# Kernel optimization log

Measured on AMD Instinct MI355X. Metric: run time of the kernel, lower is better.

The kernel has to match this reference:

```python
import jax, jax.numpy as jnp
import numpy as np

N_NODES = 100000
N_EDGES = 1600000
IN_CH, HID_CH, OUT_CH = 128, 128, 64


def _sage_conv(x, src, dst, deg_inv, W_l, b_l, W_r):
    # PyG SAGEConv (mean aggr): out = lin_l(mean_{j in N(i)} x_j) + lin_r(x_i)
    msg = x[src]                                   # [E, C_in] gather
    agg = jax.ops.segment_sum(msg, dst, num_segments=N_NODES)  # [N, C_in]
    agg = agg * deg_inv[:, None]
    return agg @ W_l.T + b_l + x @ W_r.T


def setup_inputs() -> dict:
    key = jax.random.key(0)
    ks = jax.random.split(key, 10)
    x = jax.random.normal(ks[0], (N_NODES, IN_CH), dtype=jnp.float32)
    edge_attr = jax.random.normal(ks[1], (N_EDGES, 4), dtype=jnp.float32)
    edge_index = jax.random.randint(ks[2], (2, N_EDGES), 0, N_NODES, dtype=jnp.int32)
    dims = [(IN_CH, HID_CH), (HID_CH, HID_CH), (HID_CH, OUT_CH)]
    params = {}
    for i, (cin, cout) in enumerate(dims):
        s = 1.0 / np.sqrt(cin)
        params[f"W_l{i}"] = jax.random.uniform(ks[3 + 2 * i], (cout, cin), minval=-s, maxval=s, dtype=jnp.float32)
        params[f"b_l{i}"] = jnp.zeros((cout,), dtype=jnp.float32)
        params[f"W_r{i}"] = jax.random.uniform(ks[4 + 2 * i], (cout, cin), minval=-s, maxval=s, dtype=jnp.float32)
    return {"x": x, "edge_attr": edge_attr, "edge_index": edge_index, **params}


def reference(x, edge_attr, edge_index,
              W_l0, b_l0, W_r0,
              W_l1, b_l1, W_r1,
              W_l2, b_l2, W_r2):
    src, dst = edge_index[0], edge_index[1]
    deg = jax.ops.segment_sum(jnp.ones((N_EDGES,), jnp.float32), dst, num_segments=N_NODES)
    deg_inv = 1.0 / jnp.maximum(deg, 1.0)
    layers = [(W_l0, b_l0, W_r0), (W_l1, b_l1, W_r1), (W_l2, b_l2, W_r2)]
    h = x
    for i, (Wl, bl, Wr) in enumerate(layers):
        h = _sage_conv(h, src, dst, deg_inv, Wl, bl, Wr)
        if i != len(layers) - 1:
            h = jax.nn.relu(h)
            # dropout is identity in eval mode (training=False)
    return h
```

## Files before the change

kernel.cpp:

```cpp
#include <hip/hip_runtime.h>
#include <cstdint>

#define N_NODES 100000
#define N_EDGES 1600000

constexpr int NCB = 196;
constexpr int HB  = 391;

typedef __attribute__((ext_vector_type(8))) short short8;
typedef __attribute__((ext_vector_type(4))) float f32x4;

__device__ inline uint32_t fbits(float f) { union { float f; uint32_t u; } c; c.f = f; return c.u; }
__device__ inline float bfloat(uint32_t u) { union { uint32_t u; float f; } c; c.u = u; return c.f; }

__device__ inline void bsplit(float a, short& hi, short& lo) {
    uint32_t h = fbits(a) & 0xFFFF0000u;
    float fl = a - bfloat(h);
    hi = (short)(h >> 16);
    lo = (short)(fbits(fl) >> 16);
}

__device__ inline ushort f2bf(float f) {
    uint32_t u = fbits(f);
    return (ushort)((u + 0x7FFFu + ((u >> 16) & 1u)) >> 16);
}


__global__ __launch_bounds__(256)
void hist_kernel(const int* __restrict__ dst, int* __restrict__ H) {
    __shared__ int h[NCB];
    for (int i = threadIdx.x; i < NCB; i += 256) h[i] = 0;
    __syncthreads();
    int e0 = blockIdx.x * 4096;
    #pragma unroll
    for (int it = 0; it < 16; ++it) {
        int e = e0 + it * 256 + threadIdx.x;
        if (e < N_EDGES) atomicAdd(&h[dst[e] >> 9], 1);
    }
    __syncthreads();
    for (int i = threadIdx.x; i < NCB; i += 256) H[blockIdx.x * NCB + i] = h[i];
}

__global__ __launch_bounds__(256)
void scanbase_kernel(int* __restrict__ H, int* __restrict__ boff) {
    __shared__ int tot[NCB];
    __shared__ int base[NCB + 1];
    int j = threadIdx.x;
    if (j < NCB) {
        int s = 0;
        for (int b = 0; b < HB; ++b) s += H[b * NCB + j];
        tot[j] = s;
    }
    __syncthreads();
    if (j == 0) {
        int run = 0;
        for (int k = 0; k < NCB; ++k) { base[k] = run; run += tot[k]; }
        base[NCB] = run;
    }
    __syncthreads();
    if (j <= NCB) boff[j] = base[j];
    if (j < NCB) {
        int run = base[j];
        for (int b = 0; b < HB; ++b) {
            int v = H[b * NCB + j];
            H[b * NCB + j] = run;
            run += v;
        }
    }
}

__global__ __launch_bounds__(256)
void scatter_kernel(const int* __restrict__ src, const int* __restrict__ dst,
                    const int* __restrict__ H, uint32_t* __restrict__ ebuf) {
    __shared__ int cur[NCB];
    for (int i = threadIdx.x; i < NCB; i += 256) cur[i] = H[blockIdx.x * NCB + i];
    __syncthreads();
    int e0 = blockIdx.x * 4096;
    #pragma unroll
    for (int it = 0; it < 16; ++it) {
        int e = e0 + it * 256 + threadIdx.x;
        if (e < N_EDGES) {
            int d = dst[e];
            int p = atomicAdd(&cur[d >> 9], 1);
            ebuf[p] = ((uint32_t)src[e] << 9) | (uint32_t)(d & 511);
        }
    }
}


__global__ __launch_bounds__(256)
void bucket_csr(const uint32_t* __restrict__ ebuf, const int* __restrict__ boff,
                int* __restrict__ off, float* __restrict__ dinv,
                int* __restrict__ ssrc) {
    __shared__ int deg[512];
    __shared__ int cur[512];
    __shared__ int wsum[4];
    int t = threadIdx.x, lane = t & 63, w = t >> 6;
    int j = blockIdx.x;
    int base = boff[j], end = boff[j + 1];
    int node0 = j << 9;

    deg[t] = 0; deg[t + 256] = 0;
    __syncthreads();

    for (int p = base + t; p < end; p += 256)
        atomicAdd(&deg[ebuf[p] & 511u], 1);
    __syncthreads();

    int d0 = deg[2 * t], d1 = deg[2 * t + 1];
    int s = d0 + d1;
    int incl = s;
    #pragma unroll
    for (int d = 1; d < 64; d <<= 1) {
        int u = __shfl_up(incl, d);
        if (lane >= d) incl += u;
    }
    if (lane == 63) wsum[w] = incl;
    __syncthreads();
    if (t < 4) {
        int v = wsum[t];
        int iv = v;
        #pragma unroll
        for (int d = 1; d < 4; d <<= 1) {
            int u = __shfl_up(iv, d, 4);
            if (t >= d) iv += u;
        }
        wsum[t] = iv - v;
    }
    __syncthreads();
    int ebase = wsum[w] + (incl - s);
    cur[2 * t] = ebase;
    cur[2 * t + 1] = ebase + d0;
    int n0 = node0 + 2 * t, n1 = n0 + 1;
    if (n0 < N_NODES) {
        off[n0] = base + ebase;
        dinv[n0] = 1.0f / (float)max(d0, 1);
    }
    if (n1 < N_NODES) {
        off[n1] = base + ebase + d0;
        dinv[n1] = 1.0f / (float)max(d1, 1);
    }
    if (j == 0 && t == 0) off[N_NODES] = N_EDGES;
    __syncthreads();

    for (int p = base + t; p < end; p += 256) {
        uint32_t ent = ebuf[p];
        int pos = atomicAdd(&cur[ent & 511u], 1);
        ssrc[base + pos] = (int)(ent >> 9);
    }
}


__global__ void wfrag_kernel(const float* __restrict__ W1, const float* __restrict__ W2,
                             int C1, int NCT, int ntask,
                             short* __restrict__ fhi, short* __restrict__ flo) {
    int tau = blockIdx.x * 256 + threadIdx.x;
    if (tau >= ntask) return;
    int lane = tau & 63;
    int ct = (tau >> 6) % NCT;
    int ks = (tau >> 6) / NCT;
    int col = ct * 16 + (lane & 15);
    int k = ks * 32 + (lane >> 4) * 8;
    const float* p = (col < C1) ? &W1[(size_t)col * 128 + k]
                                : &W2[(size_t)(col - C1) * 128 + k];
    short8 h8, l8;
    #pragma unroll
    for (int j = 0; j < 8; ++j) {
        short h, l;
        bsplit(p[j], h, l);
        h8[j] = h; l8[j] = l;
    }
    *reinterpret_cast<short8*>(&fhi[(size_t)tau * 8]) = h8;
    *reinterpret_cast<short8*>(&flo[(size_t)tau * 8]) = l8;
}


template<int C1, int C2>
__global__ __launch_bounds__(256)
void gemm_f32(const float* __restrict__ H, const short* __restrict__ Wfhi,
              const short* __restrict__ Wflo, const float* __restrict__ bias2,
              ushort* __restrict__ out1, ushort* __restrict__ out2) {
    constexpr int COUT = C1 + C2;
    constexpr int CT = COUT / 64;
    constexpr int NCT = COUT / 16;
    __shared__ short smem[16384];
    short* Ahi = smem;
    short* Alo = smem + 8192;
    int t = threadIdx.x;
    int l = t & 63, w = t >> 6;
    int lr = l & 15, kg = l >> 4;
    int r0 = blockIdx.x * 64;
    int c_base = w * (COUT / 4);
    const bool is1 = (c_base < C1);

    #pragma unroll
    for (int it = 0; it < 4; ++it) {
        int lin = t + it * 256;
        int row = lin >> 4, ch = lin & 15;
        float av[8];
        if (r0 + row < N_NODES) {
            const float* p = &H[(size_t)(r0 + row) * 128 + ch * 8];
            float4 v0 = *reinterpret_cast<const float4*>(p);
            float4 v1 = *reinterpret_cast<const float4*>(p + 4);
            av[0] = v0.x; av[1] = v0.y; av[2] = v0.z; av[3] = v0.w;
            av[4] = v1.x; av[5] = v1.y; av[6] = v1.z; av[7] = v1.w;
        } else {
            #pragma unroll
            for (int j = 0; j < 8; ++j) av[j] = 0.f;
        }
        short8 h8, l8;
        #pragma unroll
        for (int j = 0; j < 8; ++j) {
            short h, lo2;
            bsplit(av[j], h, lo2);
            h8[j] = h; l8[j] = lo2;
        }
        int off = row * 128 + ((ch ^ (row & 7)) << 3);
        *reinterpret_cast<short8*>(&Ahi[off]) = h8;
        *reinterpret_cast<short8*>(&Alo[off]) = l8;
    }
    __syncthreads();

    f32x4 acc[4][CT];
    #pragma unroll
    for (int m = 0; m < 4; ++m)
        #pragma unroll
        for (int c = 0; c < CT; ++c)
            acc[m][c] = (f32x4){0.f, 0.f, 0.f, 0.f};

    #pragma unroll
    for (int ks = 0; ks < 4; ++ks) {
        int ch = ks * 4 + kg;
        short8 ahi[4], alo[4];
        #pragma unroll
        for (int m = 0; m < 4; ++m) {
            int row = m * 16 + lr;
            int off = row * 128 + ((ch ^ (row & 7)) << 3);
            ahi[m] = *reinterpret_cast<const short8*>(&Ahi[off]);
            alo[m] = *reinterpret_cast<const short8*>(&Alo[off]);
        }
        short8 bhi[CT], blo[CT];
        #pragma unroll
        for (int c = 0; c < CT; ++c) {
            int ctg = w * CT + c;
            size_t fo = ((size_t)(ks * NCT + ctg) * 64 + l) * 8;
            bhi[c] = *reinterpret_cast<const short8*>(&Wfhi[fo]);
            blo[c] = *reinterpret_cast<const short8*>(&Wflo[fo]);
        }
        #pragma unroll
        for (int m = 0; m < 4; ++m)
            #pragma unroll
            for (int c = 0; c < CT; ++c) {
                acc[m][c] = __builtin_amdgcn_mfma_f32_16x16x32_bf16(ahi[m], bhi[c], acc[m][c], 0, 0, 0);
                acc[m][c] = __builtin_amdgcn_mfma_f32_16x16x32_bf16(ahi[m], blo[c], acc[m][c], 0, 0, 0);
                acc[m][c] = __builtin_amdgcn_mfma_f32_16x16x32_bf16(alo[m], bhi[c], acc[m][c], 0, 0, 0);
            }
    }

    float bb[CT];
    #pragma unroll
    for (int c = 0; c < CT; ++c) {
        int colg = c_base + c * 16 + lr;
        bb[c] = is1 ? 0.f : bias2[colg - C1];
    }
    __syncthreads();
    ushort* Ct = (ushort*)smem;
    #pragma unroll
    for (int c = 0; c < CT; ++c) {
        int seg = c_base / 16 + c;
        #pragma unroll
        for (int m = 0; m < 4; ++m)
            #pragma unroll
            for (int r = 0; r < 4; ++r) {
                int row = m * 16 + kg * 4 + r;
                int sw = seg ^ ((row >> 2) & 3);
                Ct[row * 256 + sw * 16 + lr] = f2bf(acc[m][c][r] + bb[c]);
            }
    }
    __syncthreads();
    #pragma unroll
    for (int it = 0; it < 8; ++it) {
        int lin = it * 256 + t;
        int row = lin >> 5, chk = lin & 31;
        int grow = r0 + row;
        if (grow < N_NODES) {
            int sw = (chk >> 1) ^ ((row >> 2) & 3);
            uint4 v = *reinterpret_cast<const uint4*>(&Ct[row * 256 + sw * 16 + (chk & 1) * 8]);
            if (chk < 16)
                *reinterpret_cast<uint4*>(&out1[(size_t)grow * C1 + chk * 8]) = v;
            else
                *reinterpret_cast<uint4*>(&out2[(size_t)grow * C2 + (chk - 16) * 8]) = v;
        }
    }
}


template<int C1, int C2, bool ZF32>
__global__ __launch_bounds__(256)
void gemm_bf16(const ushort* __restrict__ H, const short* __restrict__ Wfhi,
               const short* __restrict__ Wflo, const float* __restrict__ bias2,
               ushort* __restrict__ out1, void* __restrict__ out2v) {
    constexpr int COUT = C1 + C2;
    constexpr int CT = COUT / 64;
    constexpr int NCT = COUT / 16;
    constexpr int SMEM = ZF32 ? 8192 : (64 * COUT > 8192 ? 64 * COUT : 8192);
    __shared__ short smem[SMEM];
    short* A = smem;
    int t = threadIdx.x;
    int l = t & 63, w = t >> 6;
    int lr = l & 15, kg = l >> 4;
    int r0 = blockIdx.x * 64;
    int c_base = w * (COUT / 4);
    const bool is1 = (c_base < C1);

    #pragma unroll
    for (int it = 0; it < 4; ++it) {
        int lin = t + it * 256;
        int row = lin >> 4, ch = lin & 15;
        short8 v = (short8){0, 0, 0, 0, 0, 0, 0, 0};
        if (r0 + row < N_NODES)
            v = *reinterpret_cast<const short8*>(&H[(size_t)(r0 + row) * 128 + ch * 8]);
        int off = row * 128 + ((ch ^ (row & 7)) << 3);
        *reinterpret_cast<short8*>(&A[off]) = v;
    }
    __syncthreads();

    f32x4 acc[4][CT];
    #pragma unroll
    for (int m = 0; m < 4; ++m)
        #pragma unroll
        for (int c = 0; c < CT; ++c)
            acc[m][c] = (f32x4){0.f, 0.f, 0.f, 0.f};

    #pragma unroll
    for (int ks = 0; ks < 4; ++ks) {
        int ch = ks * 4 + kg;
        short8 a[4];
        #pragma unroll
        for (int m = 0; m < 4; ++m) {
            int row = m * 16 + lr;
            int off = row * 128 + ((ch ^ (row & 7)) << 3);
            a[m] = *reinterpret_cast<const short8*>(&A[off]);
        }
        short8 bhi[CT], blo[CT];
        #pragma unroll
        for (int c = 0; c < CT; ++c) {
            int ctg = w * CT + c;
            size_t fo = ((size_t)(ks * NCT + ctg) * 64 + l) * 8;
            bhi[c] = *reinterpret_cast<const short8*>(&Wfhi[fo]);
            blo[c] = *reinterpret_cast<const short8*>(&Wflo[fo]);
        }
        #pragma unroll
        for (int m = 0; m < 4; ++m)
            #pragma unroll
            for (int c = 0; c < CT; ++c) {
                acc[m][c] = __builtin_amdgcn_mfma_f32_16x16x32_bf16(a[m], bhi[c], acc[m][c], 0, 0, 0);
                acc[m][c] = __builtin_amdgcn_mfma_f32_16x16x32_bf16(a[m], blo[c], acc[m][c], 0, 0, 0);
            }
    }

    if (!ZF32) {
        float bb[CT];
        #pragma unroll
        for (int c = 0; c < CT; ++c) {
            int colg = c_base + c * 16 + lr;
            bb[c] = is1 ? 0.f : bias2[colg - C1];
        }
        __syncthreads();
        ushort* Ct = (ushort*)smem;
        #pragma unroll
        for (int c = 0; c < CT; ++c) {
            int seg = c_base / 16 + c;
            #pragma unroll
            for (int m = 0; m < 4; ++m)
                #pragma unroll
                for (int r = 0; r < 4; ++r) {
                    int row = m * 16 + kg * 4 + r;
                    int sw = seg ^ ((row >> 2) & 3);
                    Ct[row * COUT + sw * 16 + lr] = f2bf(acc[m][c][r] + bb[c]);
                }
        }
        __syncthreads();
        constexpr int CHR = COUT / 8;
        #pragma unroll
        for (int it = 0; it < 64 * CHR / 256; ++it) {
            int lin = it * 256 + t;
            int row = lin / CHR, chk = lin % CHR;
            int grow = r0 + row;
            if (grow < N_NODES) {
                int sw = (chk >> 1) ^ ((row >> 2) & 3);
                uint4 v = *reinterpret_cast<const uint4*>(&Ct[row * COUT + sw * 16 + (chk & 1) * 8]);
                if (chk < C1 / 8)
                    *reinterpret_cast<uint4*>(&out1[(size_t)grow * C1 + chk * 8]) = v;
                else
                    *reinterpret_cast<uint4*>(&((ushort*)out2v)[(size_t)grow * C2 + (chk - C1 / 8) * 8]) = v;
            }
        }
    } else {
        __syncthreads();
        ushort* Yt = (ushort*)smem;
        if (is1) {
            #pragma unroll
            for (int c = 0; c < CT; ++c) {
                int seg = c_base / 16 + c;
                #pragma unroll
                for (int m = 0; m < 4; ++m)
                    #pragma unroll
                    for (int r = 0; r < 4; ++r) {
                        int row = m * 16 + kg * 4 + r;
                        int sw = seg ^ ((row >> 2) & 3);
                        Yt[row * C1 + sw * 16 + lr] = f2bf(acc[m][c][r]);
                    }
            }
        } else {
            float* out2 = (float*)out2v;
            #pragma unroll
            for (int c = 0; c < CT; ++c) {
                int col = c_base - C1 + c * 16 + lr;
                float bbv = bias2[col];
                #pragma unroll
                for (int m = 0; m < 4; ++m)
                    #pragma unroll
                    for (int r = 0; r < 4; ++r) {
                        int row = r0 + m * 16 + kg * 4 + r;
                        if (row < N_NODES)
                            out2[(size_t)row * C2 + col] = acc[m][c][r] + bbv;
                    }
            }
        }
        __syncthreads();
        constexpr int CHR = C1 / 8;
        #pragma unroll
        for (int it = 0; it < 64 * CHR / 256; ++it) {
            int lin = it * 256 + t;
            int row = lin / CHR, chk = lin % CHR;
            int grow = r0 + row;
            if (grow < N_NODES) {
                int sw = (chk >> 1) ^ ((row >> 2) & 3);
                uint4 v = *reinterpret_cast<const uint4*>(&Yt[row * C1 + sw * 16 + (chk & 1) * 8]);
                *reinterpret_cast<uint4*>(&out1[(size_t)grow * C1 + chk * 8]) = v;
            }
        }
    }
}


template<int C, bool FINAL>
__global__ __launch_bounds__(256)
void agg_wave(const ushort* __restrict__ Y, const void* __restrict__ Zv,
              const int* __restrict__ off, const int* __restrict__ ssrc,
              const float* __restrict__ dinv, void* __restrict__ outv) {
    constexpr int NCH = C / 8;
    constexpr int ESL = 64 / NCH;
    int t = threadIdx.x, l = t & 63;
    int i = blockIdx.x * 4 + (t >> 6);
    int chunk = l & (NCH - 1);
    int eslot = l / NCH;
    int p0 = off[i], p1 = off[i + 1];

    float acc[8] = {0.f, 0.f, 0.f, 0.f, 0.f, 0.f, 0.f, 0.f};
    for (int p = p0; p < p1; p += 4 * ESL) {
        #pragma unroll
        for (int u = 0; u < 4; ++u) {
            int q = p + u * ESL + eslot;
            if (q < p1) {
                int s = ssrc[q];
                uint4 v = *reinterpret_cast<const uint4*>(&Y[(size_t)s * C + chunk * 8]);
                uint32_t wd[4] = {v.x, v.y, v.z, v.w};
                #pragma unroll
                for (int j = 0; j < 4; ++j) {
                    acc[2 * j]     += bfloat(wd[j] << 16);
                    acc[2 * j + 1] += bfloat(wd[j] & 0xFFFF0000u);
                }
            }
        }
    }
    #pragma unroll
    for (int d = NCH; d < 64; d <<= 1)
        #pragma unroll
        for (int j = 0; j < 8; ++j)
            acc[j] += __shfl_xor(acc[j], d);

    if (eslot == 0) {
        float di = dinv[i];
        float zz[8];
        if (FINAL) {
            const float* Z = (const float*)Zv;
            const float* zp = &Z[(size_t)i * C + chunk * 8];
            float4 z0 = *reinterpret_cast<const float4*>(zp);
            float4 z1 = *reinterpret_cast<const float4*>(zp + 4);
            zz[0] = z0.x; zz[1] = z0.y; zz[2] = z0.z; zz[3] = z0.w;
            zz[4] = z1.x; zz[5] = z1.y; zz[6] = z1.z; zz[7] = z1.w;
        } else {
            const ushort* Z = (const ushort*)Zv;
            uint4 zv = *reinterpret_cast<const uint4*>(&Z[(size_t)i * C + chunk * 8]);
            uint32_t wd[4] = {zv.x, zv.y, zv.z, zv.w};
            #pragma unroll
            for (int j = 0; j < 4; ++j) {
                zz[2 * j]     = bfloat(wd[j] << 16);
                zz[2 * j + 1] = bfloat(wd[j] & 0xFFFF0000u);
            }
        }
        float r[8];
        #pragma unroll
        for (int j = 0; j < 8; ++j) {
            r[j] = acc[j] * di + zz[j];
            if (!FINAL) r[j] = fmaxf(r[j], 0.f);
        }
        if (FINAL) {
            float* O = (float*)outv;
            float* op = &O[(size_t)i * C + chunk * 8];
            *reinterpret_cast<float4*>(op)     = make_float4(r[0], r[1], r[2], r[3]);
            *reinterpret_cast<float4*>(op + 4) = make_float4(r[4], r[5], r[6], r[7]);
        } else {
            ushort* O = (ushort*)outv;
            uint4 o;
            o.x = (uint32_t)f2bf(r[0]) | ((uint32_t)f2bf(r[1]) << 16);
            o.y = (uint32_t)f2bf(r[2]) | ((uint32_t)f2bf(r[3]) << 16);
            o.z = (uint32_t)f2bf(r[4]) | ((uint32_t)f2bf(r[5]) << 16);
            o.w = (uint32_t)f2bf(r[6]) | ((uint32_t)f2bf(r[7]) << 16);
            *reinterpret_cast<uint4*>(&O[(size_t)i * C + chunk * 8]) = o;
        }
    }
}


extern "C" void kernel_launch(void* const* d_in, const int* in_sizes, int n_in,
                              void* d_out, int out_size, void* d_ws, size_t ws_size,
                              hipStream_t stream) {
    const float* x   = (const float*)d_in[0];
    const int*   ei  = (const int*)d_in[2];
    const float* Wl0 = (const float*)d_in[3];
    const float* bl0 = (const float*)d_in[4];
    const float* Wr0 = (const float*)d_in[5];
    const float* Wl1 = (const float*)d_in[6];
    const float* bl1 = (const float*)d_in[7];
    const float* Wr1 = (const float*)d_in[8];
    const float* Wl2 = (const float*)d_in[9];
    const float* bl2 = (const float*)d_in[10];
    const float* Wr2 = (const float*)d_in[11];
    float* out = (float*)d_out;

    char* ws = (char*)d_ws;
    int*      H    = (int*)(ws + 0);
    int*      boff = (int*)(ws + (size_t)(384 << 10));
    int*      off  = (int*)(ws + (size_t)(512 << 10));
    float*    dinv = (float*)(ws + (size_t)(960 << 10));
    uint32_t* ebuf = (uint32_t*)(ws + (size_t)(1400 << 10));
    int*      ssrc = (int*)(ws + (size_t)(1400 << 10) + (size_t)(7 << 20));
    short* w0hi = (short*)(ws + (size_t)(16 << 20));
    short* w0lo = w0hi + 32768;
    short* w1hi = w0lo + 32768;
    short* w1lo = w1hi + 32768;
    short* w2hi = w1lo + 32768;
    short* w2lo = w2hi + 16384;
    ushort* Ybf = (ushort*)(ws + (size_t)(18 << 20));
    ushort* Zbf = (ushort*)(ws + (size_t)(44 << 20));
    ushort* Hbf = (ushort*)(ws + (size_t)(70 << 20));

    const int* srcp = ei;
    const int* dstp = ei + N_EDGES;

    hist_kernel<<<HB, 256, 0, stream>>>(dstp, H);
    scanbase_kernel<<<1, 256, 0, stream>>>(H, boff);
    scatter_kernel<<<HB, 256, 0, stream>>>(srcp, dstp, H, ebuf);
    bucket_csr<<<NCB, 256, 0, stream>>>(ebuf, boff, off, dinv, ssrc);

    wfrag_kernel<<<16, 256, 0, stream>>>(Wl0, Wr0, 128, 16, 4096, w0hi, w0lo);
    wfrag_kernel<<<16, 256, 0, stream>>>(Wl1, Wr1, 128, 16, 4096, w1hi, w1lo);
    wfrag_kernel<<<8, 256, 0, stream>>>(Wl2, Wr2, 64, 8, 2048, w2hi, w2lo);

    int ggrid = (N_NODES + 63) / 64;
    int wgrid = (N_NODES + 3) / 4;

    gemm_f32<128, 128><<<ggrid, 256, 0, stream>>>(x, w0hi, w0lo, bl0, Ybf, Zbf);
    agg_wave<128, false><<<wgrid, 256, 0, stream>>>(Ybf, Zbf, off, ssrc, dinv, Hbf);

    gemm_bf16<128, 128, false><<<ggrid, 256, 0, stream>>>(Hbf, w1hi, w1lo, bl1, Ybf, Zbf);
    agg_wave<128, false><<<wgrid, 256, 0, stream>>>(Ybf, Zbf, off, ssrc, dinv, Hbf);

    gemm_bf16<64, 64, true><<<ggrid, 256, 0, stream>>>(Hbf, w2hi, w2lo, bl2, Ybf, (void*)Zbf);
    agg_wave<64, true><<<wgrid, 256, 0, stream>>>(Ybf, (const void*)Zbf, off, ssrc, dinv, out);
}
```

Baseline: 347.0 us.

## Split aggregation over channel halves with software-pipelined gather loads

```diff
diff --git a/kernel.cpp b/kernel.cpp
--- a/kernel.cpp
+++ b/kernel.cpp
@@ -6,6 +6,7 @@
 
 constexpr int NCB = 196;
 constexpr int HB  = 391;
+constexpr int NBK = N_NODES / 4;
 
 typedef __attribute__((ext_vector_type(8))) short short8;
 typedef __attribute__((ext_vector_type(4))) float f32x4;
@@ -23,6 +24,11 @@
 __device__ inline ushort f2bf(float f) {
     uint32_t u = fbits(f);
     return (ushort)((u + 0x7FFFu + ((u >> 16) & 1u)) >> 16);
+}
+
+__device__ inline void acc_word(uint32_t w, float& lo, float& hi) {
+    lo += bfloat(w << 16);
+    hi += bfloat(w & 0xFFFF0000u);
 }
 
 
@@ -445,55 +451,65 @@
 }
 
 
-template<int C, bool FINAL>
-__global__ __launch_bounds__(256)
-void agg_wave(const ushort* __restrict__ Y, const void* __restrict__ Zv,
-              const int* __restrict__ off, const int* __restrict__ ssrc,
-              const float* __restrict__ dinv, void* __restrict__ outv) {
-    constexpr int NCH = C / 8;
-    constexpr int ESL = 64 / NCH;
+template<bool FINAL>
+__global__ __launch_bounds__(256)
+void agg8(const ushort* __restrict__ Y, const void* __restrict__ Zv,
+          const int* __restrict__ off, const int* __restrict__ ssrc,
+          const float* __restrict__ dinv, void* __restrict__ outv, int RSE) {
     int t = threadIdx.x, l = t & 63;
-    int i = blockIdx.x * 4 + (t >> 6);
-    int chunk = l & (NCH - 1);
-    int eslot = l / NCH;
+    int bid = blockIdx.x;
+    int nb = bid % NBK;
+    int half = bid / NBK;
+    int i = nb * 4 + (t >> 6);
+    int chunk = l & 7;
+    int eslot = l >> 3;
+    int cbase = half * 64 + chunk * 8;
+    const ushort* Yb = Y + cbase;
+
     int p0 = off[i], p1 = off[i + 1];
-
     float acc[8] = {0.f, 0.f, 0.f, 0.f, 0.f, 0.f, 0.f, 0.f};
-    for (int p = p0; p < p1; p += 4 * ESL) {
-        #pragma unroll
-        for (int u = 0; u < 4; ++u) {
-            int q = p + u * ESL + eslot;
-            if (q < p1) {
-                int s = ssrc[q];
-                uint4 v = *reinterpret_cast<const uint4*>(&Y[(size_t)s * C + chunk * 8]);
-                uint32_t wd[4] = {v.x, v.y, v.z, v.w};
-                #pragma unroll
-                for (int j = 0; j < 4; ++j) {
-                    acc[2 * j]     += bfloat(wd[j] << 16);
-                    acc[2 * j + 1] += bfloat(wd[j] & 0xFFFF0000u);
-                }
-            }
-        }
-    }
-    #pragma unroll
-    for (int d = NCH; d < 64; d <<= 1)
+
+    #define LDQ(q, v, a)  { a = (q) < p1; if (a) { int s_ = ssrc[q]; \
+        v = *reinterpret_cast<const uint4*>(&Yb[(size_t)s_ * RSE]); } }
+    #define ACCU(v) { acc_word(v.x, acc[0], acc[1]); acc_word(v.y, acc[2], acc[3]); \
+                      acc_word(v.z, acc[4], acc[5]); acc_word(v.w, acc[6], acc[7]); }
+
+    uint4 c0, c1;
+    bool a0, a1;
+    LDQ(p0 + eslot, c0, a0)
+    LDQ(p0 + 8 + eslot, c1, a1)
+    for (int p = p0 + 16; p < p1; p += 16) {
+        uint4 n0, n1;
+        bool b0, b1;
+        LDQ(p + eslot, n0, b0)
+        LDQ(p + 8 + eslot, n1, b1)
+        if (a0) ACCU(c0)
+        if (a1) ACCU(c1)
+        c0 = n0; c1 = n1; a0 = b0; a1 = b1;
+    }
+    if (a0) ACCU(c0)
+    if (a1) ACCU(c1)
+    #undef LDQ
+    #undef ACCU
+
+    #pragma unroll
+    for (int d = 8; d < 64; d <<= 1)
         #pragma unroll
         for (int j = 0; j < 8; ++j)
             acc[j] += __shfl_xor(acc[j], d);
 
     if (eslot == 0) {
         float di = dinv[i];
+        size_t eo = (size_t)i * RSE + cbase;
         float zz[8];
         if (FINAL) {
-            const float* Z = (const float*)Zv;
-            const float* zp = &Z[(size_t)i * C + chunk * 8];
+            const float* zp = (const float*)Zv + eo;
             float4 z0 = *reinterpret_cast<const float4*>(zp);
             float4 z1 = *reinterpret_cast<const float4*>(zp + 4);
             zz[0] = z0.x; zz[1] = z0.y; zz[2] = z0.z; zz[3] = z0.w;
             zz[4] = z1.x; zz[5] = z1.y; zz[6] = z1.z; zz[7] = z1.w;
         } else {
-            const ushort* Z = (const ushort*)Zv;
-            uint4 zv = *reinterpret_cast<const uint4*>(&Z[(size_t)i * C + chunk * 8]);
+            uint4 zv = *reinterpret_cast<const uint4*>((const ushort*)Zv + eo);
             uint32_t wd[4] = {zv.x, zv.y, zv.z, zv.w};
             #pragma unroll
             for (int j = 0; j < 4; ++j) {
@@ -508,18 +524,16 @@
             if (!FINAL) r[j] = fmaxf(r[j], 0.f);
         }
         if (FINAL) {
-            float* O = (float*)outv;
-            float* op = &O[(size_t)i * C + chunk * 8];
+            float* op = (float*)outv + eo;
             *reinterpret_cast<float4*>(op)     = make_float4(r[0], r[1], r[2], r[3]);
             *reinterpret_cast<float4*>(op + 4) = make_float4(r[4], r[5], r[6], r[7]);
         } else {
-            ushort* O = (ushort*)outv;
             uint4 o;
             o.x = (uint32_t)f2bf(r[0]) | ((uint32_t)f2bf(r[1]) << 16);
             o.y = (uint32_t)f2bf(r[2]) | ((uint32_t)f2bf(r[3]) << 16);
             o.z = (uint32_t)f2bf(r[4]) | ((uint32_t)f2bf(r[5]) << 16);
             o.w = (uint32_t)f2bf(r[6]) | ((uint32_t)f2bf(r[7]) << 16);
-            *reinterpret_cast<uint4*>(&O[(size_t)i * C + chunk * 8]) = o;
+            *reinterpret_cast<uint4*>((ushort*)outv + eo) = o;
         }
     }
 }
@@ -571,14 +585,13 @@
     wfrag_kernel<<<8, 256, 0, stream>>>(Wl2, Wr2, 64, 8, 2048, w2hi, w2lo);
 
     int ggrid = (N_NODES + 63) / 64;
-    int wgrid = (N_NODES + 3) / 4;
 
     gemm_f32<128, 128><<<ggrid, 256, 0, stream>>>(x, w0hi, w0lo, bl0, Ybf, Zbf);
-    agg_wave<128, false><<<wgrid, 256, 0, stream>>>(Ybf, Zbf, off, ssrc, dinv, Hbf);
+    agg8<false><<<2 * NBK, 256, 0, stream>>>(Ybf, Zbf, off, ssrc, dinv, Hbf, 128);
 
     gemm_bf16<128, 128, false><<<ggrid, 256, 0, stream>>>(Hbf, w1hi, w1lo, bl1, Ybf, Zbf);
-    agg_wave<128, false><<<wgrid, 256, 0, stream>>>(Ybf, Zbf, off, ssrc, dinv, Hbf);
+    agg8<false><<<2 * NBK, 256, 0, stream>>>(Ybf, Zbf, off, ssrc, dinv, Hbf, 128);
 
     gemm_bf16<64, 64, true><<<ggrid, 256, 0, stream>>>(Hbf, w2hi, w2lo, bl2, Ybf, (void*)Zbf);
-    agg_wave<64, true><<<wgrid, 256, 0, stream>>>(Ybf, (const void*)Zbf, off, ssrc, dinv, out);
-}
+    agg8<true><<<NBK, 256, 0, stream>>>(Ybf, (const void*)Zbf, off, ssrc, dinv, out, 64);
+}
```

New measurement: 362.9 us. 4.6% more time.
